# Optimization experiments

Measured on AMD Instinct MI355X. Metric: run time of the kernel, lower is better.

The kernel has to match this reference:

```python
import jax, jax.numpy as jnp
import numpy as np

B, S, D = 2, 2048, 2048
H, HKV, HD = 16, 4, 128
GROUPS = H // HKV
SCALE = HD ** -0.5
ROPE_THETA = 10000.0
NEG = -1e9


def _rope_cos_sin():
    inv_freq = 1.0 / (ROPE_THETA ** (jnp.arange(0, HD, 2, dtype=jnp.float32) / HD))  # [HD/2]
    pos = jnp.arange(S, dtype=jnp.float32)
    freqs = pos[:, None] * inv_freq[None, :]            # [S, HD/2]
    emb = jnp.concatenate([freqs, freqs], axis=-1)      # [S, HD]
    cos = jnp.broadcast_to(jnp.cos(emb)[None], (B, S, HD))
    sin = jnp.broadcast_to(jnp.sin(emb)[None], (B, S, HD))
    return cos, sin


def setup_inputs() -> dict:
    key = jax.random.key(0)
    ks = jax.random.split(key, 5)
    hidden_states = jax.random.normal(ks[0], (B, S, D), dtype=jnp.float32)
    cos, sin = _rope_cos_sin()
    causal = jnp.where(jnp.arange(S)[:, None] >= jnp.arange(S)[None, :], 0.0, NEG).astype(jnp.float32)
    attn_mask = jnp.broadcast_to(causal[None, None], (B, 1, S, S))
    wq = jax.random.normal(ks[1], (H * HD, D), dtype=jnp.float32) * (D ** -0.5)
    wk = jax.random.normal(ks[2], (HKV * HD, D), dtype=jnp.float32) * (D ** -0.5)
    wv = jax.random.normal(ks[3], (HKV * HD, D), dtype=jnp.float32) * (D ** -0.5)
    wo = jax.random.normal(ks[4], (D, H * HD), dtype=jnp.float32) * (D ** -0.5)
    return {"hidden_states": hidden_states, "cos": cos, "sin": sin,
            "attn_mask": attn_mask, "wq": wq, "wk": wk, "wv": wv, "wo": wo}


def _rotate_half(x):
    x1, x2 = x[..., : HD // 2], x[..., HD // 2:]
    return jnp.concatenate([-x2, x1], axis=-1)


def reference(hidden_states, cos, sin, attn_mask, wq, wk, wv, wo):
    # projections (torch Linear: x @ W.T), reshape to [B, heads, S, HD]
    q = (hidden_states @ wq.T).reshape(B, S, H, HD).transpose(0, 2, 1, 3)
    k = (hidden_states @ wk.T).reshape(B, S, HKV, HD).transpose(0, 2, 1, 3)
    v = (hidden_states @ wv.T).reshape(B, S, HKV, HD).transpose(0, 2, 1, 3)
    # RoPE (cos/sin broadcast over head dim)
    c = cos[:, None, :, :]
    s = sin[:, None, :, :]
    q = q * c + _rotate_half(q) * s
    k = k * c + _rotate_half(k) * s
    # GQA: repeat each kv head GROUPS times consecutively (matches repeat_kv)
    k = jnp.repeat(k, GROUPS, axis=1)
    v = jnp.repeat(v, GROUPS, axis=1)
    logits = jnp.einsum('bhqd,bhkd->bhqk', q, k) * SCALE + attn_mask
    w = jax.nn.softmax(logits.astype(jnp.float32), axis=-1).astype(q.dtype)
    out = jnp.einsum('bhqk,bhkd->bhqd', w, v)            # [B,H,S,HD]
    out = out.transpose(0, 2, 1, 3).reshape(B, S, H * HD)
    return out @ wo.T
```

## Files before the change

kernel.cpp:

```cpp
#include <hip/hip_runtime.h>

typedef __attribute__((ext_vector_type(8))) short bf16x8;
typedef __attribute__((ext_vector_type(4))) float f32x4;
typedef __attribute__((ext_vector_type(16))) float f32x16;
typedef __attribute__((ext_vector_type(8))) unsigned short u16x8;
typedef __attribute__((ext_vector_type(4))) unsigned u32x4;
typedef unsigned short u16;

#define GLOBAL_AS __attribute__((address_space(1)))
#define LDS_AS __attribute__((address_space(3)))

#define S_ 2048
#define SMK_ 0.12751741406106783f

static __device__ __forceinline__ u16 f2bf(float f) {
  unsigned u = __builtin_bit_cast(unsigned, f);
  u += 0x7fffu + ((u >> 16) & 1u);
  return (u16)(u >> 16);
}
static __device__ __forceinline__ float bf2f(u16 h) {
  return __builtin_bit_cast(float, ((unsigned)h) << 16);
}
static __device__ __forceinline__ float exp2_raw(float x) {
  float r; asm("v_exp_f32 %0, %1" : "=v"(r) : "v"(x)); return r;
}
static __device__ __forceinline__ unsigned cvtpk(float lo, float hi_) {
  unsigned r; asm("v_cvt_pk_bf16_f32 %0, %1, %2" : "=v"(r) : "v"(lo), "v"(hi_)); return r;
}

__global__ __launch_bounds__(256)
void cvt_all(const float* __restrict__ h, const float* __restrict__ wq,
             const float* __restrict__ wk, const float* __restrict__ wv,
             const float* __restrict__ wo, u16* __restrict__ Xbf,
             u16* __restrict__ Wqkv, u16* __restrict__ Wo) {
  const int bid = blockIdx.x;
  const float* src; u16* dst; long base;
  if (bid < 4096)      { src = h;  dst = Xbf;            base = (long)bid * 2048; }
  else if (bid < 6144) { src = wq; dst = Wqkv;           base = (long)(bid - 4096) * 2048; }
  else if (bid < 6656) { src = wk; dst = Wqkv + 4194304; base = (long)(bid - 6144) * 2048; }
  else if (bid < 7168) { src = wv; dst = Wqkv + 5242880; base = (long)(bid - 6656) * 2048; }
  else                 { src = wo; dst = Wo;             base = (long)(bid - 7168) * 2048; }
  const long i = base + (long)threadIdx.x * 8;
  f32x4 a = *(const f32x4*)(src + i);
  f32x4 b = *(const f32x4*)(src + i + 4);
  u16x8 o;
  o[0] = f2bf(a[0]); o[1] = f2bf(a[1]); o[2] = f2bf(a[2]); o[3] = f2bf(a[3]);
  o[4] = f2bf(b[0]); o[5] = f2bf(b[1]); o[6] = f2bf(b[2]); o[7] = f2bf(b[3]);
  *(u16x8*)(dst + i) = o;
}

template <bool BF16OUT>
__global__ __launch_bounds__(256)
void gemm_bt(const u16* __restrict__ A, const u16* __restrict__ Bw,
             void* __restrict__ Cp, int M, int N, int K) {
  __shared__ u16 As[128 * 64];
  __shared__ u16 Bs[128 * 64];
  const int tid = threadIdx.x;
  const int wave = tid >> 6, lane = tid & 63;
  const int fr = lane & 15, fg = lane >> 4;
  const int wm = (wave >> 1) * 64, wn = (wave & 1) * 64;
  const long rowA = (long)blockIdx.y * 128;
  const long rowB = (long)blockIdx.x * 128;

  f32x4 acc[4][4] = {};

  for (int k0 = 0; k0 < K; k0 += 64) {
    __syncthreads();
#pragma unroll
    for (int c = 0; c < 4; ++c) {
      const int base = (wave * 4 + c) * 1024;
      const int off = base + lane * 16;
      const int r = off >> 7;
      const int kc = (off & 127) >> 1;
      __builtin_amdgcn_global_load_lds(
          (GLOBAL_AS void*)(A + (rowA + r) * (long)K + k0 + kc),
          (LDS_AS void*)(As + (base >> 1)), 16, 0, 0);
      __builtin_amdgcn_global_load_lds(
          (GLOBAL_AS void*)(Bw + (rowB + r) * (long)K + k0 + kc),
          (LDS_AS void*)(Bs + (base >> 1)), 16, 0, 0);
    }
    __syncthreads();
#pragma unroll
    for (int ks = 0; ks < 2; ++ks) {
      bf16x8 af[4], bfr[4];
#pragma unroll
      for (int i = 0; i < 4; ++i) {
        af[i]  = *(const bf16x8*)&As[(wm + i * 16 + fr) * 64 + ks * 32 + fg * 8];
        bfr[i] = *(const bf16x8*)&Bs[(wn + i * 16 + fr) * 64 + ks * 32 + fg * 8];
      }
#pragma unroll
      for (int i = 0; i < 4; ++i)
#pragma unroll
        for (int j = 0; j < 4; ++j)
          acc[i][j] = __builtin_amdgcn_mfma_f32_16x16x32_bf16(af[i], bfr[j], acc[i][j], 0, 0, 0);
    }
  }
#pragma unroll
  for (int i = 0; i < 4; ++i)
#pragma unroll
    for (int j = 0; j < 4; ++j)
#pragma unroll
      for (int r = 0; r < 4; ++r) {
        const long row = rowA + wm + i * 16 + fg * 4 + r;
        const long col = rowB + wn + j * 16 + fr;
        if (BF16OUT) ((u16*)Cp)[row * N + col] = f2bf(acc[i][j][r]);
        else         ((float*)Cp)[row * N + col] = acc[i][j][r];
      }
}

__global__ __launch_bounds__(256)
void rope_rearrange(const u16* __restrict__ QKV, const float* __restrict__ cosb,
                    const float* __restrict__ sinb, u16* __restrict__ Qr,
                    u16* __restrict__ Kr) {
  const int m = blockIdx.x;
  const int b = m >> 11, s = m & 2047;
  const int t = threadIdx.x;
  const u16* row = QKV + (long)m * 3072;
  const float* cp = cosb + (long)m * 128;
  const float* sp = sinb + (long)m * 128;
#pragma unroll
  for (int i = 0; i < 4; ++i) {
    const int idx = i * 256 + t;
    const int h = idx >> 6, d = idx & 63;
    const float x1 = bf2f(row[h * 128 + d]);
    const float x2 = bf2f(row[h * 128 + d + 64]);
    const float c = cp[d], sv = sp[d];
    const long o = ((long)(b * 16 + h) * S_ + s) * 128 + d;
    Qr[o] = f2bf(x1 * c - x2 * sv);
    Qr[o + 64] = f2bf(x2 * c + x1 * sv);
  }
  {
    const int h = t >> 6, d = t & 63;
    const float x1 = bf2f(row[2048 + h * 128 + d]);
    const float x2 = bf2f(row[2048 + h * 128 + d + 64]);
    const float c = cp[d], sv = sp[d];
    const long o = ((long)(b * 4 + h) * S_ + s) * 128 + d;
    Kr[o] = f2bf((x1 * c - x2 * sv) * SMK_);
    Kr[o + 64] = f2bf((x2 * c + x1 * sv) * SMK_);
  }
}

__global__ __launch_bounds__(256)
void transpose_v(const u16* __restrict__ QKV, u16* __restrict__ Vt) {
  __shared__ u16 t[32][33];
  const int s0 = blockIdx.x * 32, d0 = blockIdx.y * 32;
  const int bk = blockIdx.z;
  const int b = bk >> 2, kh = bk & 3;
  const int tx = threadIdx.x & 31, ty = threadIdx.x >> 5;
  const u16* src = QKV + 2560 + (long)kh * 128;
#pragma unroll
  for (int i = 0; i < 4; ++i) {
    const int sl = ty + i * 8;
    t[sl][tx] = src[(long)(b * S_ + s0 + sl) * 3072 + d0 + tx];
  }
  __syncthreads();
  u16* dst = Vt + (long)(b * 4 + kh) * 128 * S_;
#pragma unroll
  for (int i = 0; i < 4; ++i) {
    const int dl = ty + i * 8;
    dst[(long)(d0 + dl) * S_ + s0 + tx] = t[tx][dl];
  }
}

struct PA2 { bf16x8 a, b; };
static __device__ __forceinline__ PA2 pack_half(const f32x16 s) {
  PA2 out;
#pragma unroll
  for (int ks2 = 0; ks2 < 2; ++ks2) {
    const int rb = ks2 * 8;
    unsigned w0 = cvtpk(s[rb + 0], s[rb + 1]);
    unsigned w1 = cvtpk(s[rb + 2], s[rb + 3]);
    unsigned w2 = cvtpk(s[rb + 4], s[rb + 5]);
    unsigned w3 = cvtpk(s[rb + 6], s[rb + 7]);
    asm("v_permlane32_swap_b32 %0, %1" : "+v"(w0), "+v"(w2));
    asm("v_permlane32_swap_b32 %0, %1" : "+v"(w1), "+v"(w3));
    u32x4 pw; pw[0] = w0; pw[1] = w1; pw[2] = w2; pw[3] = w3;
    if (ks2 == 0) out.a = __builtin_bit_cast(bf16x8, pw);
    else          out.b = __builtin_bit_cast(bf16x8, pw);
  }
  return out;
}

template <int NH>
static __device__ __forceinline__ void attn_tile(
    const u16* __restrict__ Ks, const u16* __restrict__ Vs,
    const bf16x8 (&qf)[8], f32x16 (&acc)[4], float& m_run, float& l_run,
    const int kv0, const int qwmin, const int qg, const int l31,
    const int hi, const int r7) {
  f32x16 s[NH];
#pragma unroll
  for (int hh = 0; hh < NH; ++hh) s[hh] = (f32x16){};
  __builtin_amdgcn_s_setprio(1);
#pragma unroll
  for (int ds = 0; ds < 8; ++ds) {
    const int ch = ((2 * ds + hi) ^ r7) << 3;
#pragma unroll
    for (int hh = 0; hh < NH; ++hh) {
      const bf16x8 ka = *(const bf16x8*)&Ks[(hh * 32 + l31) * 128 + ch];
      s[hh] = __builtin_amdgcn_mfma_f32_32x32x16_bf16(ka, qf[ds], s[hh], 0, 0, 0);
    }
  }
  __builtin_amdgcn_s_setprio(0);

  if (kv0 + NH * 32 - 1 > qwmin) {
#pragma unroll
    for (int hh = 0; hh < NH; ++hh)
#pragma unroll
      for (int r = 0; r < 16; ++r) {
        const int cr = (r & 3) + 8 * (r >> 2) + 4 * hi;
        if (kv0 + hh * 32 + cr > qg) s[hh][r] = -3.0e38f;
      }
  }

  float mx = s[0][0];
#pragma unroll
  for (int hh = 0; hh < NH; ++hh)
#pragma unroll
    for (int r = 0; r < 16; ++r) mx = fmaxf(mx, s[hh][r]);
  mx = fmaxf(mx, __shfl_xor(mx, 32));

  if (__any(mx > m_run + 8.0f)) {
    const float mn = fmaxf(m_run, mx);
    const float scq = exp2_raw(m_run - mn);
    m_run = mn; l_run *= scq;
#pragma unroll
    for (int r = 0; r < 16; ++r) {
      const int cr = (r & 3) + 8 * (r >> 2) + 4 * hi;
      const float sr = __shfl(scq, cr);
      acc[0][r] *= sr; acc[1][r] *= sr; acc[2][r] *= sr; acc[3][r] *= sr;
    }
  }

  float rs = 0.f;
#pragma unroll
  for (int hh = 0; hh < NH; ++hh)
#pragma unroll
    for (int r = 0; r < 16; ++r) { s[hh][r] = exp2_raw(s[hh][r] - m_run); rs += s[hh][r]; }
  rs += __shfl_xor(rs, 32);
  l_run += rs;

  bf16x8 pa[2 * NH];
#pragma unroll
  for (int hh = 0; hh < NH; ++hh) {
    const PA2 p = pack_half(s[hh]);
    pa[2 * hh] = p.a; pa[2 * hh + 1] = p.b;
  }
  __builtin_amdgcn_s_setprio(1);
#pragma unroll
  for (int nj = 0; nj < 4; ++nj) {
    const int vrow = (nj * 32 + l31) * 64;
#pragma unroll
    for (int ks = 0; ks < 2 * NH; ++ks) {
      const bf16x8 vf = *(const bf16x8*)&Vs[vrow + (((2 * ks + hi) ^ r7) << 3)];
      acc[nj] = __builtin_amdgcn_mfma_f32_32x32x16_bf16(pa[ks], vf, acc[nj], 0, 0, 0);
    }
  }
  __builtin_amdgcn_s_setprio(0);
}

#define NUNITS 1024
__global__ __launch_bounds__(128)
void attn_fwd(const u16* __restrict__ Qr, const u16* __restrict__ Kr,
              const u16* __restrict__ Vt, u16* __restrict__ Att,
              unsigned* __restrict__ ctr) {
  __shared__ u16 Ks[64 * 128];
  __shared__ u16 Vs[128 * 64];
  __shared__ unsigned s_uid;

  const int tid = threadIdx.x, wave = tid >> 6, lane = tid & 63;
  const int l31 = lane & 31, hi = lane >> 5, r7 = lane & 7;

  for (;;) {
    __syncthreads();
    if (tid == 0) s_uid = atomicAdd(ctr, 1u);
    __syncthreads();
    const unsigned uid = s_uid;
    if (uid >= NUNITS) break;

    const int qt = 31 - (int)(uid >> 5);
    const int bh = uid & 31;
    const int b = bh >> 4, h = bh & 15;
    const int kh = h >> 2;
    const int qwmin = qt * 64 + wave * 32;

    const u16* Qb = Qr + (long)(b * 16 + h) * S_ * 128;
    const u16* Kb = Kr + (long)(b * 4 + kh) * S_ * 128;
    const u16* Vg = Vt + (long)(b * 4 + kh) * 128 * (long)S_;

    bf16x8 qf[8];
    const u16* qrow = Qb + (long)(qwmin + l31) * 128 + hi * 8;
#pragma unroll
    for (int ds = 0; ds < 8; ++ds) qf[ds] = *(const bf16x8*)(qrow + ds * 16);

    f32x16 acc[4] = {};
    float m_run = -1e30f, l_run = 0.f;
    const int qg = qwmin + l31;

    const int ntiles = qt + 1;
    for (int t = 0; t < ntiles; ++t) {
      const int kv0 = t * 64;
      __syncthreads();
#pragma unroll
      for (int c = 0; c < 8; ++c) {
        const int slab = wave * 8 + c;
        const int offu = slab * 512 + lane * 8;
        const int kvl = offu >> 7;
        const int kc = ((offu >> 3) & 15) ^ (kvl & 7);
        __builtin_amdgcn_global_load_lds(
            (GLOBAL_AS void*)(Kb + (long)(kv0 + kvl) * 128 + kc * 8),
            (LDS_AS void*)(Ks + slab * 512), 16, 0, 0);
        const int dr = offu >> 6;
        const int vc = ((offu >> 3) & 7) ^ (dr & 7);
        __builtin_amdgcn_global_load_lds(
            (GLOBAL_AS void*)(Vg + (long)dr * S_ + kv0 + vc * 8),
            (LDS_AS void*)(Vs + slab * 512), 16, 0, 0);
      }
      __syncthreads();

      if (kv0 + 32 <= qwmin + 31)
        attn_tile<2>(Ks, Vs, qf, acc, m_run, l_run, kv0, qwmin, qg, l31, hi, r7);
      else if (kv0 <= qwmin + 31)
        attn_tile<1>(Ks, Vs, qf, acc, m_run, l_run, kv0, qwmin, qg, l31, hi, r7);
    }

    const float inv = 1.0f / l_run;
#pragma unroll
    for (int r = 0; r < 16; ++r) {
      const int cr = (r & 3) + 8 * (r >> 2) + 4 * hi;
      const float ir = __shfl(inv, cr);
      const long orow = ((long)b * S_ + qt * 64 + wave * 32 + cr) * 2048 + h * 128 + l31;
      Att[orow]      = f2bf(acc[0][r] * ir);
      Att[orow + 32] = f2bf(acc[1][r] * ir);
      Att[orow + 64] = f2bf(acc[2][r] * ir);
      Att[orow + 96] = f2bf(acc[3][r] * ir);
    }
  }
}

extern "C" void kernel_launch(void* const* d_in, const int* in_sizes, int n_in,
                              void* d_out, int out_size, void* d_ws, size_t ws_size,
                              hipStream_t stream) {
  const float* hidden = (const float*)d_in[0];
  const float* cosb = (const float*)d_in[1];
  const float* sinb = (const float*)d_in[2];
  const float* wq = (const float*)d_in[4];
  const float* wk = (const float*)d_in[5];
  const float* wv = (const float*)d_in[6];
  const float* wo = (const float*)d_in[7];
  float* out = (float*)d_out;

  u16* Xbf  = (u16*)d_ws;
  u16* Wqkv = Xbf + 8388608;
  u16* Wo   = Wqkv + 6291456;
  u16* QKV  = Wo + 4194304;
  u16* Qr   = QKV + 12582912;
  u16* Kr   = Qr + 8388608;
  u16* Vtp  = Kr + 2097152;
  u16* Att  = Xbf;
  if (ws_size < (size_t)44040192 * 2) return;

  cvt_all<<<dim3(9216), dim3(256), 0, stream>>>(hidden, wq, wk, wv, wo, Xbf, Wqkv, Wo);
  gemm_bt<true><<<dim3(24, 32), dim3(256), 0, stream>>>(Xbf, Wqkv, (void*)QKV, 4096, 3072, 2048);
  rope_rearrange<<<dim3(4096), dim3(256), 0, stream>>>(QKV, cosb, sinb, Qr, Kr);
  transpose_v<<<dim3(64, 4, 8), dim3(256), 0, stream>>>(QKV, Vtp);
  hipMemsetAsync((void*)Wqkv, 0, 4, stream);
  attn_fwd<<<dim3(768), dim3(128), 0, stream>>>(Qr, Kr, Vtp, Att, (unsigned*)Wqkv);
  gemm_bt<false><<<dim3(16, 32), dim3(256), 0, stream>>>(Att, Wo, (void*)out, 4096, 2048, 2048);
}
```

Before: 254.9 us.

## Replace GEMM with 256-row tiled, 4-stage pipelined, swizzled-LDS kernel

New measurement: 224.6 us. -11.9%, faster.

```diff
diff --git a/kernel.cpp b/kernel.cpp
--- a/kernel.cpp
+++ b/kernel.cpp
@@ -49,62 +49,124 @@
   *(u16x8*)(dst + i) = o;
 }
 
-template <bool BF16OUT>
-__global__ __launch_bounds__(256)
-void gemm_bt(const u16* __restrict__ A, const u16* __restrict__ Bw,
+template <int NJ, bool BF16OUT>
+__global__ __launch_bounds__(512, 2)
+void gemm256(const u16* __restrict__ A, const u16* __restrict__ Bw,
              void* __restrict__ Cp, int M, int N, int K) {
-  __shared__ u16 As[128 * 64];
-  __shared__ u16 Bs[128 * 64];
+  __shared__ u16 LA[4][2][4096];
+  __shared__ u16 LB[4][NJ / 2][4096];
+
   const int tid = threadIdx.x;
   const int wave = tid >> 6, lane = tid & 63;
   const int fr = lane & 15, fg = lane >> 4;
-  const int wm = (wave >> 1) * 64, wn = (wave & 1) * 64;
-  const long rowA = (long)blockIdx.y * 128;
-  const long rowB = (long)blockIdx.x * 128;
-
-  f32x4 acc[4][4] = {};
-
-  for (int k0 = 0; k0 < K; k0 += 64) {
-    __syncthreads();
-#pragma unroll
-    for (int c = 0; c < 4; ++c) {
-      const int base = (wave * 4 + c) * 1024;
-      const int off = base + lane * 16;
-      const int r = off >> 7;
-      const int kc = (off & 127) >> 1;
-      __builtin_amdgcn_global_load_lds(
-          (GLOBAL_AS void*)(A + (rowA + r) * (long)K + k0 + kc),
-          (LDS_AS void*)(As + (base >> 1)), 16, 0, 0);
-      __builtin_amdgcn_global_load_lds(
-          (GLOBAL_AS void*)(Bw + (rowB + r) * (long)K + k0 + kc),
-          (LDS_AS void*)(Bs + (base >> 1)), 16, 0, 0);
-    }
-    __syncthreads();
-#pragma unroll
-    for (int ks = 0; ks < 2; ++ks) {
-      bf16x8 af[4], bfr[4];
-#pragma unroll
-      for (int i = 0; i < 4; ++i) {
-        af[i]  = *(const bf16x8*)&As[(wm + i * 16 + fr) * 64 + ks * 32 + fg * 8];
-        bfr[i] = *(const bf16x8*)&Bs[(wn + i * 16 + fr) * 64 + ks * 32 + fg * 8];
-      }
-#pragma unroll
-      for (int i = 0; i < 4; ++i)
-#pragma unroll
-        for (int j = 0; j < 4; ++j)
-          acc[i][j] = __builtin_amdgcn_mfma_f32_16x16x32_bf16(af[i], bfr[j], acc[i][j], 0, 0, 0);
-    }
-  }
-#pragma unroll
-  for (int i = 0; i < 4; ++i)
-#pragma unroll
-    for (int j = 0; j < 4; ++j)
+  const int wm = (wave >> 2) * 128;
+  const int wn = (wave & 3) * (NJ * 16);
+  const long rowA = (long)blockIdx.y * 256;
+  const long rowB = (long)blockIdx.x * (NJ * 64);
+
+  const int srow = tid >> 2;
+  const int sc8 = (tid & 3) ^ (srow & 3);
+  const int wbase = wave * 512;
+
+  const int nt = K >> 5;
+
+  f32x4 acc[8][NJ] = {};
+
+#define STAGE_A(pt)                                                          \
+  {                                                                          \
+    const int _b = (pt) & 3;                                                 \
+    const long _k = (long)(pt) * 32 + sc8 * 8;                               \
+    __builtin_amdgcn_global_load_lds(                                        \
+        (GLOBAL_AS void*)(A + (rowA + srow) * K + _k),                       \
+        (LDS_AS void*)(&LA[_b][0][wbase]), 16, 0, 0);                        \
+    __builtin_amdgcn_global_load_lds(                                        \
+        (GLOBAL_AS void*)(A + (rowA + 128 + srow) * K + _k),                 \
+        (LDS_AS void*)(&LA[_b][1][wbase]), 16, 0, 0);                        \
+  }
+#define STAGE_B(pt)                                                          \
+  {                                                                          \
+    const int _b = (pt) & 3;                                                 \
+    const long _k = (long)(pt) * 32 + sc8 * 8;                               \
+    __builtin_amdgcn_global_load_lds(                                        \
+        (GLOBAL_AS void*)(Bw + (rowB + srow) * K + _k),                      \
+        (LDS_AS void*)(&LB[_b][0][wbase]), 16, 0, 0);                        \
+    if (NJ == 4)                                                             \
+      __builtin_amdgcn_global_load_lds(                                      \
+          (GLOBAL_AS void*)(Bw + (rowB + 128 + srow) * K + _k),              \
+          (LDS_AS void*)(&LB[_b][NJ / 2 - 1][wbase]), 16, 0, 0);             \
+  }
+
+  STAGE_A(0); STAGE_B(0);
+  STAGE_A(1); STAGE_B(1);
+  STAGE_A(2); STAGE_B(2);
+
+  for (int t = 0; t < nt; ++t) {
+    const int rem = nt - 1 - t;
+    if (NJ == 4) {
+      if (rem >= 2)      asm volatile("s_waitcnt vmcnt(8)" ::: "memory");
+      else if (rem == 1) asm volatile("s_waitcnt vmcnt(4)" ::: "memory");
+      else               asm volatile("s_waitcnt vmcnt(0)" ::: "memory");
+    } else {
+      if (rem >= 2)      asm volatile("s_waitcnt vmcnt(6)" ::: "memory");
+      else if (rem == 1) asm volatile("s_waitcnt vmcnt(3)" ::: "memory");
+      else               asm volatile("s_waitcnt vmcnt(0)" ::: "memory");
+    }
+    __builtin_amdgcn_s_barrier();
+
+    const u16* Ah = LA[t & 3][wm >> 7];
+    const u16* Bh = LB[t & 3][NJ == 4 ? (wn >> 7) : 0];
+    const bool pf = (t + 3) < nt;
+
+    bf16x8 af0[4], bfv[NJ];
+#pragma unroll
+    for (int mi = 0; mi < 4; ++mi) {
+      const int rl = mi * 16 + fr;
+      af0[mi] = *(const bf16x8*)&Ah[rl * 32 + ((fg ^ (rl & 3)) << 3)];
+    }
+#pragma unroll
+    for (int nj = 0; nj < NJ; ++nj) {
+      const int rb = (wn & 127) + nj * 16 + fr;
+      bfv[nj] = *(const bf16x8*)&Bh[rb * 32 + ((fg ^ (rb & 3)) << 3)];
+    }
+    if (pf) STAGE_A(t + 3);
+    __builtin_amdgcn_s_setprio(1);
+#pragma unroll
+    for (int mi = 0; mi < 4; ++mi)
+#pragma unroll
+      for (int nj = 0; nj < NJ; ++nj)
+        acc[mi][nj] = __builtin_amdgcn_mfma_f32_16x16x32_bf16(af0[mi], bfv[nj], acc[mi][nj], 0, 0, 0);
+    __builtin_amdgcn_s_setprio(0);
+
+    bf16x8 af1[4];
+#pragma unroll
+    for (int mi = 0; mi < 4; ++mi) {
+      const int rl = 64 + mi * 16 + fr;
+      af1[mi] = *(const bf16x8*)&Ah[rl * 32 + ((fg ^ (rl & 3)) << 3)];
+    }
+    if (pf) STAGE_B(t + 3);
+    __builtin_amdgcn_s_setprio(1);
+#pragma unroll
+    for (int mi = 0; mi < 4; ++mi)
+#pragma unroll
+      for (int nj = 0; nj < NJ; ++nj)
+        acc[4 + mi][nj] = __builtin_amdgcn_mfma_f32_16x16x32_bf16(af1[mi], bfv[nj], acc[4 + mi][nj], 0, 0, 0);
+    __builtin_amdgcn_s_setprio(0);
+
+    __builtin_amdgcn_s_barrier();
+  }
+#undef STAGE_A
+#undef STAGE_B
+
+#pragma unroll
+  for (int mi = 0; mi < 8; ++mi)
+#pragma unroll
+    for (int nj = 0; nj < NJ; ++nj)
 #pragma unroll
       for (int r = 0; r < 4; ++r) {
-        const long row = rowA + wm + i * 16 + fg * 4 + r;
-        const long col = rowB + wn + j * 16 + fr;
-        if (BF16OUT) ((u16*)Cp)[row * N + col] = f2bf(acc[i][j][r]);
-        else         ((float*)Cp)[row * N + col] = acc[i][j][r];
+        const long row = rowA + wm + mi * 16 + fg * 4 + r;
+        const long col = rowB + wn + nj * 16 + fr;
+        if (BF16OUT) ((u16*)Cp)[row * N + col] = f2bf(acc[mi][nj][r]);
+        else         ((float*)Cp)[row * N + col] = acc[mi][nj][r];
       }
 }
 
@@ -360,10 +422,10 @@
   if (ws_size < (size_t)44040192 * 2) return;
 
   cvt_all<<<dim3(9216), dim3(256), 0, stream>>>(hidden, wq, wk, wv, wo, Xbf, Wqkv, Wo);
-  gemm_bt<true><<<dim3(24, 32), dim3(256), 0, stream>>>(Xbf, Wqkv, (void*)QKV, 4096, 3072, 2048);
+  gemm256<4, true><<<dim3(12, 16), dim3(512), 0, stream>>>(Xbf, Wqkv, (void*)QKV, 4096, 3072, 2048);
   rope_rearrange<<<dim3(4096), dim3(256), 0, stream>>>(QKV, cosb, sinb, Qr, Kr);
   transpose_v<<<dim3(64, 4, 8), dim3(256), 0, stream>>>(QKV, Vtp);
   hipMemsetAsync((void*)Wqkv, 0, 4, stream);
   attn_fwd<<<dim3(768), dim3(128), 0, stream>>>(Qr, Kr, Vtp, Att, (unsigned*)Wqkv);
-  gemm_bt<false><<<dim3(16, 32), dim3(256), 0, stream>>>(Att, Wo, (void*)out, 4096, 2048, 2048);
-}
+  gemm256<2, false><<<dim3(16, 16), dim3(512), 0, stream>>>(Att, Wo, (void*)out, 4096, 2048, 2048);
+}
```
